# Performance work log

Hardware: AMD Instinct MI355X
Metric: run time of the kernel (lower is better)

The kernel has to match this reference:

```python
import jax, jax.numpy as jnp
import numpy as np
import math

B = 1048576
BG_RES = 512
NUM_LEVELS = 2
POWER = 4
MIPNOISE = 0.5
INIT_VAL = -2.0


def cube_face_uv(v):
    # v: [N,3] direction vectors. OpenGL cubemap face convention
    # (faces: 0:+x 1:-x 2:+y 3:-y 4:+z 5:-z), as used by nvdiffrast 'cube'.
    x, y, z = v[:, 0], v[:, 1], v[:, 2]
    ax, ay, az = jnp.abs(x), jnp.abs(y), jnp.abs(z)
    is_x = (ax >= ay) & (ax >= az)
    is_y = (~is_x) & (ay >= az)
    face = jnp.where(is_x, jnp.where(x >= 0, 0, 1),
                     jnp.where(is_y, jnp.where(y >= 0, 2, 3),
                               jnp.where(z >= 0, 4, 5))).astype(jnp.int32)
    ma = jnp.where(is_x, ax, jnp.where(is_y, ay, az))
    sc = jnp.where(is_x, jnp.where(x >= 0, -z, z),
                   jnp.where(is_y, x, jnp.where(z >= 0, x, -x)))
    tc = jnp.where(is_x, -y, jnp.where(is_y, jnp.where(y >= 0, z, -z), -y))
    u = 0.5 * (sc / ma + 1.0)
    t = 0.5 * (tc / ma + 1.0)
    return face, u, t


def build_pyramid(tex):
    # tex: [6,R,R,3] -> list of 2x2 box-filtered mips down to 1x1 (nvdiffrast style)
    levels = [tex]
    t = tex
    while t.shape[1] > 1:
        R = t.shape[1]
        t = t.reshape(6, R // 2, 2, R // 2, 2, 3).mean(axis=(2, 4))
        levels.append(t)
    return levels


def bilinear(tex, face, u, v):
    # tex: [6,R,R,3]; face/u/v: [N]. Clamp-to-edge bilinear per selected face.
    R = tex.shape[1]
    x = u * R - 0.5
    y = v * R - 0.5
    x0f = jnp.floor(x); y0f = jnp.floor(y)
    fx = (x - x0f)[:, None]; fy = (y - y0f)[:, None]
    x0 = jnp.clip(x0f.astype(jnp.int32), 0, R - 1)
    y0 = jnp.clip(y0f.astype(jnp.int32), 0, R - 1)
    x1 = jnp.clip(x0f.astype(jnp.int32) + 1, 0, R - 1)
    y1 = jnp.clip(y0f.astype(jnp.int32) + 1, 0, R - 1)
    flat = tex.reshape(6 * R * R, 3)
    base = face * (R * R)
    g00 = flat[base + y0 * R + x0]
    g01 = flat[base + y0 * R + x1]
    g10 = flat[base + y1 * R + x0]
    g11 = flat[base + y1 * R + x1]
    return ((1 - fx) * (1 - fy) * g00 + fx * (1 - fy) * g01 +
            (1 - fx) * fy * g10 + fx * fy * g11)


def sample_cubemap(tex6, face, u, v, mip):
    # trilinear: bilinear in two adjacent mips, lerp by fractional mip level
    levels = build_pyramid(tex6)
    lmax = float(len(levels) - 1)
    m = jnp.clip(mip, 0.0, lmax)
    out = jnp.zeros((face.shape[0], 3), tex6.dtype)
    for l, t in enumerate(levels):
        wl = jnp.clip(1.0 - jnp.abs(m - l), 0.0, 1.0)  # (1-f)/f trilinear weights
        out = out + wl[:, None] * bilinear(t, face, u, v)
    return out


def setup_inputs() -> dict:
    key = jax.random.key(0)
    k1, k2, k3, k4, k5 = jax.random.split(key, 5)
    viewdirs = jax.random.normal(k1, (B, 3), dtype=jnp.float32)
    viewdirs = viewdirs / jnp.linalg.norm(viewdirs, axis=-1, keepdims=True)
    saSample = jax.random.normal(k2, (B,), dtype=jnp.float32)
    noise_u = jax.random.uniform(k3, (B,), dtype=jnp.float32)
    # parameters (init_val*ones/(num_levels-i) in torch; perturbed for nontrivial grads)
    bg_mat0 = (INIT_VAL * jnp.ones((1, 6, 128, 128, 3), jnp.float32)
               + 0.1 * jax.random.normal(k4, (1, 6, 128, 128, 3), jnp.float32))
    bg_mat1 = (INIT_VAL / 2.0 * jnp.ones((1, 6, 512, 512, 3), jnp.float32)
               + 0.1 * jax.random.normal(k5, (1, 6, 512, 512, 3), jnp.float32))
    return {
        "viewdirs": viewdirs,
        "saSample": saSample,
        "noise_u": noise_u,
        "bg_mat0": bg_mat0,
        "bg_mat1": bg_mat1,
        "brightness": jnp.asarray(0.0, jnp.float32),
        "mul": jnp.asarray(1.0, jnp.float32),
        "mipbias": jnp.asarray(0.5, jnp.float32),
    }


def reference(viewdirs, saSample, noise_u, bg_mat0, bg_mat1, brightness, mul, mipbias):
    h = w = BG_RES  # from bg_mats[-1]
    # sa2mip
    distortion = 1.0 / jnp.max(jnp.abs(viewdirs), axis=-1)  # 1/||u||_inf
    saTexel = distortion / h / w
    miplevel = ((saSample - jnp.log(saTexel)) / math.log(POWER) / 2.0
                + mipbias + MIPNOISE * noise_u)
    miplevel = jnp.maximum(miplevel, 0.0)

    face, u, t = cube_face_uv(viewdirs)
    sumemb = sample_cubemap(bg_mat0[0], face, u, t, miplevel)  # mip 1 (128)
    sumemb = sumemb + sample_cubemap(bg_mat1[0], face, u, t, miplevel)  # mip 0 (512)

    # activation == 'identity' branch: exp(x).clip(0.01, 1000)
    img = jnp.clip(jnp.exp(jnp.clip(brightness, -1.0, 2.0) + mul * sumemb), 0.01, 1000.0)
    return img
```

## Files before the change

kernel.cpp:

```cpp
#include <hip/hip_runtime.h>
#include <hip/hip_bf16.h>
#include <math.h>


#define NPYR1_4 524286

__device__ __constant__ int OFFS0[7] = {0, 24576, 30720, 32256, 32640, 32736, 32760};
__device__ __constant__ int OFFS1[9] = {0, 393216, 491520, 516096, 522240,
                                        523776, 524160, 524256, 524280};
static const int H_OFFS0[7] = {0, 24576, 30720, 32256, 32640, 32736, 32760};
static const int H_OFFS1[9] = {0, 393216, 491520, 516096, 522240,
                               523776, 524160, 524256, 524280};

struct PyrArgs {
    const void* src;
    float4* dst[5];
    int R;
    int tpf;
    int T;
    int nlev;
    int rgba;
};

__global__ __launch_bounds__(256) void pyr_kernel(PyrArgs a0, PyrArgs a1, int split) {
    __shared__ float4 A[32 * 32];
    __shared__ float4 Bb[16 * 16];

    PyrArgs a = (blockIdx.x < (unsigned)split) ? a0 : a1;
    int bid = (blockIdx.x < (unsigned)split) ? blockIdx.x : blockIdx.x - split;

    const int tpf = a.tpf;
    const int face = bid / (tpf * tpf);
    const int tif = bid - face * tpf * tpf;
    const int ty = tif / tpf, tx = tif - (tif / tpf) * tpf;
    const int T = a.T, R = a.R;
    const int tid = threadIdx.x;
    const int baseY = ty * T, baseX = tx * T;

    const int total = T * T;
    if (a.rgba) {
        const float4* src = (const float4*)a.src;
        for (int idx = tid; idx < total; idx += 256) {
            int r = idx / T, c = idx - (idx / T) * T;
            A[r * T + c] = src[(size_t)(face * R + baseY + r) * R + baseX + c];
        }
    } else {
        const float* src = (const float*)a.src;
        for (int idx = tid; idx < total; idx += 256) {
            int r = idx / T, c = idx - (idx / T) * T;
            const float* p = src + ((size_t)(face * R + baseY + r) * R + baseX + c) * 3;
            A[r * T + c] = make_float4(p[0], p[1], p[2], 0.f);
        }
    }
    __syncthreads();

    float4* cur = A;
    float4* nxt = Bb;
    int curT = T;
    for (int l = 0; l < a.nlev; ++l) {
        const int nT = curT >> 1;
        const int Rg = R >> (l + 1);
        const int tb = T >> (l + 1);
        float4* dst = a.dst[l];
        const int n = nT * nT;
        for (int idx = tid; idx < n; idx += 256) {
            int ly = idx / nT, lx = idx - (idx / nT) * nT;
            float4 q00 = cur[(2 * ly) * curT + 2 * lx];
            float4 q01 = cur[(2 * ly) * curT + 2 * lx + 1];
            float4 q10 = cur[(2 * ly + 1) * curT + 2 * lx];
            float4 q11 = cur[(2 * ly + 1) * curT + 2 * lx + 1];
            float4 s = make_float4(0.25f * (q00.x + q01.x + q10.x + q11.x),
                                   0.25f * (q00.y + q01.y + q10.y + q11.y),
                                   0.25f * (q00.z + q01.z + q10.z + q11.z), 0.f);
            nxt[ly * nT + lx] = s;
            dst[(size_t)(face * Rg + ty * tb + ly) * Rg + tx * tb + lx] = s;
        }
        __syncthreads();
        float4* tmp = cur; cur = nxt; nxt = tmp;
        curT = nT;
    }
}

__device__ __forceinline__ void bilin4(const float4* __restrict__ tex, int R,
                                       int face, float u, float v, float o[3]) {
    float xf = u * (float)R - 0.5f;
    float yf = v * (float)R - 0.5f;
    float x0f = floorf(xf), y0f = floorf(yf);
    float fx = xf - x0f, fy = yf - y0f;
    int xi = (int)x0f, yi = (int)y0f;
    int x0 = min(max(xi, 0), R - 1);
    int x1 = min(max(xi + 1, 0), R - 1);
    int y0 = min(max(yi, 0), R - 1);
    int y1 = min(max(yi + 1, 0), R - 1);
    const float4* base = tex + (size_t)face * R * R;
    float4 p00 = base[y0 * R + x0];
    float4 p01 = base[y0 * R + x1];
    float4 p10 = base[y1 * R + x0];
    float4 p11 = base[y1 * R + x1];
    float w00 = (1.f - fx) * (1.f - fy);
    float w01 = fx * (1.f - fy);
    float w10 = (1.f - fx) * fy;
    float w11 = fx * fy;
    o[0] = w00 * p00.x + w01 * p01.x + w10 * p10.x + w11 * p11.x;
    o[1] = w00 * p00.y + w01 * p01.y + w10 * p10.y + w11 * p11.y;
    o[2] = w00 * p00.z + w01 * p01.z + w10 * p10.z + w11 * p11.z;
}

__device__ __forceinline__ void bilin3(const float* __restrict__ tex, int R,
                                       int face, float u, float v, float o[3]) {
    float xf = u * (float)R - 0.5f;
    float yf = v * (float)R - 0.5f;
    float x0f = floorf(xf), y0f = floorf(yf);
    float fx = xf - x0f, fy = yf - y0f;
    int xi = (int)x0f, yi = (int)y0f;
    int x0 = min(max(xi, 0), R - 1);
    int x1 = min(max(xi + 1, 0), R - 1);
    int y0 = min(max(yi, 0), R - 1);
    int y1 = min(max(yi + 1, 0), R - 1);
    const float* base = tex + (size_t)face * R * R * 3;
    const float* p00 = base + (y0 * R + x0) * 3;
    const float* p01 = base + (y0 * R + x1) * 3;
    const float* p10 = base + (y1 * R + x0) * 3;
    const float* p11 = base + (y1 * R + x1) * 3;
    float w00 = (1.f - fx) * (1.f - fy);
    float w01 = fx * (1.f - fy);
    float w10 = (1.f - fx) * fy;
    float w11 = fx * fy;
#pragma unroll
    for (int c = 0; c < 3; ++c)
        o[c] = w00 * p00[c] + w01 * p01[c] + w10 * p10[c] + w11 * p11[c];
}

__device__ __forceinline__ void sample_pyr(const float* __restrict__ base_tex,
                                           const float4* __restrict__ pyr,
                                           const int* offs, int lmax, int R0,
                                           int face, float u, float v, float mip,
                                           float o[3]) {
    float m = fminf(fmaxf(mip, 0.f), (float)lmax);
    float l0f = floorf(m);
    int l0 = (int)l0f;
    float f = m - l0f;
    float c0[3];
    if (l0 == 0)
        bilin3(base_tex, R0, face, u, v, c0);
    else
        bilin4(pyr + offs[l0 - 1], R0 >> l0, face, u, v, c0);
    if (f > 0.f && l0 < lmax) {
        float c1[3];
        bilin4(pyr + offs[l0], R0 >> (l0 + 1), face, u, v, c1);
        float w0 = 1.f - f;
#pragma unroll
        for (int c = 0; c < 3; ++c) o[c] = w0 * c0[c] + f * c1[c];
    } else {
#pragma unroll
        for (int c = 0; c < 3; ++c) o[c] = c0[c];
    }
}

__global__ __launch_bounds__(256) void sample_kernel(
    const float* __restrict__ vd, const float* __restrict__ sa,
    const float* __restrict__ nu, const float* __restrict__ tex0,
    const float* __restrict__ tex1, const float* __restrict__ sb,
    const float* __restrict__ sm, const float* __restrict__ smb,
    const float4* __restrict__ pyr0, const float4* __restrict__ pyr1,
    float* __restrict__ out, int n) {
    int i = blockIdx.x * 256 + threadIdx.x;
    if (i >= n) return;

    float x = vd[3 * i + 0];
    float y = vd[3 * i + 1];
    float z = vd[3 * i + 2];
    float ax = fabsf(x), ay = fabsf(y), az = fabsf(z);

    bool is_x = (ax >= ay) && (ax >= az);
    bool is_y = (!is_x) && (ay >= az);

    int face;
    float ma, sc, tc;
    if (is_x) {
        face = (x >= 0.f) ? 0 : 1;
        ma = ax;
        sc = (x >= 0.f) ? -z : z;
        tc = -y;
    } else if (is_y) {
        face = (y >= 0.f) ? 2 : 3;
        ma = ay;
        sc = x;
        tc = (y >= 0.f) ? z : -z;
    } else {
        face = (z >= 0.f) ? 4 : 5;
        ma = az;
        sc = (z >= 0.f) ? x : -x;
        tc = -y;
    }
    float u = 0.5f * (sc / ma + 1.f);
    float t = 0.5f * (tc / ma + 1.f);

    float distortion = 1.f / ma;
    float saTexel = distortion / 512.f / 512.f;
    float mip = (sa[i] - logf(saTexel)) / 1.3862943611198906f / 2.0f +
                smb[0] + 0.5f * nu[i];
    mip = fmaxf(mip, 0.f);

    float s0[3], s1[3];
    sample_pyr(tex0, pyr0, OFFS0, 7, 128, face, u, t, mip, s0);
    sample_pyr(tex1, pyr1, OFFS1, 9, 512, face, u, t, mip, s1);

    float b = fminf(fmaxf(sb[0], -1.f), 2.f);
    float mul = sm[0];
#pragma unroll
    for (int c = 0; c < 3; ++c) {
        float e = expf(b + mul * (s0[c] + s1[c]));
        out[3 * i + c] = fminf(fmaxf(e, 0.01f), 1000.f);
    }
}

extern "C" void kernel_launch(void* const* d_in, const int* in_sizes, int n_in,
                              void* d_out, int out_size, void* d_ws, size_t ws_size,
                              hipStream_t stream) {
    const float* vd = (const float*)d_in[0];
    const float* sa = (const float*)d_in[1];
    const float* nu = (const float*)d_in[2];
    const float* tex0 = (const float*)d_in[3];
    const float* tex1 = (const float*)d_in[4];
    const float* br = (const float*)d_in[5];
    const float* mu = (const float*)d_in[6];
    const float* mb = (const float*)d_in[7];
    float* out = (float*)d_out;

    float4* pyr1 = (float4*)d_ws;
    float4* pyr0 = pyr1 + NPYR1_4;

    const int B = in_sizes[1];

    PyrArgs a0{}, a1{};
    a0.src = tex1; a0.R = 512; a0.tpf = 16; a0.T = 32; a0.nlev = 5; a0.rgba = 0;
    for (int l = 0; l < 5; ++l) a0.dst[l] = pyr1 + H_OFFS1[l];
    a1.src = tex0; a1.R = 128; a1.tpf = 4; a1.T = 32; a1.nlev = 5; a1.rgba = 0;
    for (int l = 0; l < 5; ++l) a1.dst[l] = pyr0 + H_OFFS0[l];
    int split1 = 6 * 16 * 16;
    int grid1 = split1 + 6 * 4 * 4;
    hipLaunchKernelGGL(pyr_kernel, dim3(grid1), dim3(256), 0, stream, a0, a1, split1);

    PyrArgs b0{}, b1{};
    b0.src = pyr1 + H_OFFS1[4]; b0.R = 16; b0.tpf = 1; b0.T = 16; b0.nlev = 4; b0.rgba = 1;
    for (int l = 0; l < 4; ++l) b0.dst[l] = pyr1 + H_OFFS1[5 + l];
    b1.src = pyr0 + H_OFFS0[4]; b1.R = 4; b1.tpf = 1; b1.T = 4; b1.nlev = 2; b1.rgba = 1;
    for (int l = 0; l < 2; ++l) b1.dst[l] = pyr0 + H_OFFS0[5 + l];
    hipLaunchKernelGGL(pyr_kernel, dim3(12), dim3(256), 0, stream, b0, b1, 6);

    int grid = (B + 255) / 256;
    hipLaunchKernelGGL(sample_kernel, dim3(grid), dim3(256), 0, stream,
                       vd, sa, nu, tex0, tex1, br, mu, mb, pyr0, pyr1, out, B);
}
```

Measured before the change: 139.9 us.

## Precompute packed 2x2 footprint texels for coarse mip levels

Adds a kernel that, for mip levels 3 and coarser, stores each bilinear 2x2 neighbourhood (with edge clamping baked in) as 12 contiguous floats. Sampling at those levels then needs three adjacent float4 loads instead of four scattered float4 gathers. The point is fewer memory transactions per sample for coarse levels. The cost is an extra kernel launch and extra workspace, while fine levels keep the old path.

Measured after the change: 141.3 us. Within noise of the previous version (+1.0%).

```diff
diff --git a/kernel.cpp b/kernel.cpp
--- a/kernel.cpp
+++ b/kernel.cpp
@@ -1,9 +1,10 @@
 #include <hip/hip_runtime.h>
-#include <hip/hip_bf16.h>
 #include <math.h>
 
 
 #define NPYR1_4 524286
+#define FPB 557052
+#define NFP 36780
 
 __device__ __constant__ int OFFS0[7] = {0, 24576, 30720, 32256, 32640, 32736, 32760};
 __device__ __constant__ int OFFS1[9] = {0, 393216, 491520, 516096, 522240,
@@ -11,6 +12,17 @@
 static const int H_OFFS0[7] = {0, 24576, 30720, 32256, 32640, 32736, 32760};
 static const int H_OFFS1[9] = {0, 393216, 491520, 516096, 522240,
                                523776, 524160, 524256, 524280};
+
+__device__ __constant__ int FPO1C[7] = {0, 25350, 31884, 33618, 34104, 34254, 34308};
+__device__ __constant__ int FPO0C[5] = {34332, 36066, 36552, 36702, 36756};
+
+__device__ __constant__ int C_SEG_START[13] = {0, 25350, 31884, 33618, 34104, 34254,
+                                               34308, 34332, 36066, 36552, 36702,
+                                               36756, 36780};
+__device__ __constant__ int C_SEG_R[12] = {64, 32, 16, 8, 4, 2, 1, 16, 8, 4, 2, 1};
+__device__ __constant__ int C_SEG_SRC[12] = {491520, 516096, 522240, 523776, 524160,
+                                             524256, 524280, 555006, 556542, 556926,
+                                             557022, 557046};
 
 struct PyrArgs {
     const void* src;
@@ -81,6 +93,57 @@
     }
 }
 
+__global__ __launch_bounds__(256) void fpify_kernel(const float4* __restrict__ ws4,
+                                                    float4* __restrict__ fp4) {
+    int t = blockIdx.x * 256 + threadIdx.x;
+    if (t >= NFP) return;
+    int s = 0;
+#pragma unroll
+    for (int k = 1; k <= 12; ++k)
+        if (t >= C_SEG_START[k]) s = k;
+    int local = t - C_SEG_START[s];
+    int R = C_SEG_R[s];
+    int per1 = R + 1;
+    int per = per1 * per1;
+    int face = local / per;
+    int rem = local - face * per;
+    int j = rem / per1;
+    int i = rem - j * per1;
+    const float4* fb = ws4 + C_SEG_SRC[s] + (size_t)face * R * R;
+    int x0 = max(i - 1, 0), x1 = min(i, R - 1);
+    int y0 = max(j - 1, 0), y1 = min(j, R - 1);
+    float4 q00 = fb[y0 * R + x0];
+    float4 q01 = fb[y0 * R + x1];
+    float4 q10 = fb[y1 * R + x0];
+    float4 q11 = fb[y1 * R + x1];
+    size_t d = (size_t)t * 4;
+    fp4[d]     = make_float4(q00.x, q00.y, q00.z, q01.x);
+    fp4[d + 1] = make_float4(q01.y, q01.z, q10.x, q10.y);
+    fp4[d + 2] = make_float4(q10.z, q11.x, q11.y, q11.z);
+}
+
+__device__ __forceinline__ void sample_level_fp(const float4* __restrict__ fp, int R,
+                                                int face, float u, float v, float o[3]) {
+    float xf = u * (float)R - 0.5f;
+    float yf = v * (float)R - 0.5f;
+    float x0f = floorf(xf), y0f = floorf(yf);
+    float fx = xf - x0f, fy = yf - y0f;
+    int i = min(max((int)x0f + 1, 0), R);
+    int j = min(max((int)y0f + 1, 0), R);
+    int per1 = R + 1;
+    size_t base = (size_t)((face * per1 + j) * per1 + i) * 4;
+    float4 A  = fp[base];
+    float4 Bq = fp[base + 1];
+    float4 C  = fp[base + 2];
+    float w00 = (1.f - fx) * (1.f - fy);
+    float w01 = fx * (1.f - fy);
+    float w10 = (1.f - fx) * fy;
+    float w11 = fx * fy;
+    o[0] = w00 * A.x + w01 * A.w + w10 * Bq.z + w11 * C.y;
+    o[1] = w00 * A.y + w01 * Bq.x + w10 * Bq.w + w11 * C.z;
+    o[2] = w00 * A.z + w01 * Bq.y + w10 * C.x + w11 * C.w;
+}
+
 __device__ __forceinline__ void bilin4(const float4* __restrict__ tex, int R,
                                        int face, float u, float v, float o[3]) {
     float xf = u * (float)R - 0.5f;
@@ -133,7 +196,10 @@
 
 __device__ __forceinline__ void sample_pyr(const float* __restrict__ base_tex,
                                            const float4* __restrict__ pyr,
-                                           const int* offs, int lmax, int R0,
+                                           const int* offs,
+                                           const float4* __restrict__ fp4,
+                                           const int* fpoffs,
+                                           int lmax, int R0,
                                            int face, float u, float v, float mip,
                                            float o[3]) {
     float m = fminf(fmaxf(mip, 0.f), (float)lmax);
@@ -141,13 +207,19 @@
     int l0 = (int)l0f;
     float f = m - l0f;
     float c0[3];
-    if (l0 == 0)
+    if (l0 >= 3)
+        sample_level_fp(fp4 + (size_t)fpoffs[l0 - 3] * 4, R0 >> l0, face, u, v, c0);
+    else if (l0 == 0)
         bilin3(base_tex, R0, face, u, v, c0);
     else
         bilin4(pyr + offs[l0 - 1], R0 >> l0, face, u, v, c0);
     if (f > 0.f && l0 < lmax) {
         float c1[3];
-        bilin4(pyr + offs[l0], R0 >> (l0 + 1), face, u, v, c1);
+        int l1 = l0 + 1;
+        if (l1 >= 3)
+            sample_level_fp(fp4 + (size_t)fpoffs[l1 - 3] * 4, R0 >> l1, face, u, v, c1);
+        else
+            bilin4(pyr + offs[l1 - 1], R0 >> l1, face, u, v, c1);
         float w0 = 1.f - f;
 #pragma unroll
         for (int c = 0; c < 3; ++c) o[c] = w0 * c0[c] + f * c1[c];
@@ -163,7 +235,7 @@
     const float* __restrict__ tex1, const float* __restrict__ sb,
     const float* __restrict__ sm, const float* __restrict__ smb,
     const float4* __restrict__ pyr0, const float4* __restrict__ pyr1,
-    float* __restrict__ out, int n) {
+    const float4* __restrict__ fp4, float* __restrict__ out, int n) {
     int i = blockIdx.x * 256 + threadIdx.x;
     if (i >= n) return;
 
@@ -203,8 +275,8 @@
     mip = fmaxf(mip, 0.f);
 
     float s0[3], s1[3];
-    sample_pyr(tex0, pyr0, OFFS0, 7, 128, face, u, t, mip, s0);
-    sample_pyr(tex1, pyr1, OFFS1, 9, 512, face, u, t, mip, s1);
+    sample_pyr(tex0, pyr0, OFFS0, fp4, FPO0C, 7, 128, face, u, t, mip, s0);
+    sample_pyr(tex1, pyr1, OFFS1, fp4, FPO1C, 9, 512, face, u, t, mip, s1);
 
     float b = fminf(fmaxf(sb[0], -1.f), 2.f);
     float mul = sm[0];
@@ -230,6 +302,7 @@
 
     float4* pyr1 = (float4*)d_ws;
     float4* pyr0 = pyr1 + NPYR1_4;
+    float4* fp4 = pyr1 + FPB;
 
     const int B = in_sizes[1];
 
@@ -249,7 +322,10 @@
     for (int l = 0; l < 2; ++l) b1.dst[l] = pyr0 + H_OFFS0[5 + l];
     hipLaunchKernelGGL(pyr_kernel, dim3(12), dim3(256), 0, stream, b0, b1, 6);
 
+    hipLaunchKernelGGL(fpify_kernel, dim3((NFP + 255) / 256), dim3(256), 0, stream,
+                       (const float4*)d_ws, fp4);
+
     int grid = (B + 255) / 256;
     hipLaunchKernelGGL(sample_kernel, dim3(grid), dim3(256), 0, stream,
-                       vd, sa, nu, tex0, tex1, br, mu, mb, pyr0, pyr1, out, B);
-}
+                       vd, sa, nu, tex0, tex1, br, mu, mb, pyr0, pyr1, fp4, out, B);
+}
```
